# Optimization experiments

Measured on AMD Instinct MI355X. Metric: run time of the kernel, lower is better.

## Reference

```python
import jax, jax.numpy as jnp
import numpy as np

D_MODEL = 1024
NUM_HEADS = 16
D_K = D_MODEL // NUM_HEADS  # 64


def setup_inputs() -> dict:
    key = jax.random.key(0)
    k1, k2, k3, k4, k5 = jax.random.split(key, 5)
    scale = 1.0 / np.sqrt(D_MODEL)
    x = jax.random.normal(k1, (2, 8192, D_MODEL), dtype=jnp.float32)
    W_qkv = jax.random.normal(k2, (D_MODEL, 3 * D_MODEL), dtype=jnp.float32) * scale
    b_qkv = jax.random.normal(k3, (3 * D_MODEL,), dtype=jnp.float32) * 0.01
    W_out = jax.random.normal(k4, (D_MODEL, D_MODEL), dtype=jnp.float32) * scale
    b_out = jax.random.normal(k5, (D_MODEL,), dtype=jnp.float32) * 0.01
    return {"x": x, "W_qkv": W_qkv, "b_qkv": b_qkv, "W_out": W_out, "b_out": b_out}


def reference(x, W_qkv, b_qkv, W_out, b_out):
    B, S, _ = x.shape
    # qkv: [B, S, 3*d_model] -> reshape [B, S, H, 3*d_k] (matches torch reshape:
    # head h owns contiguous slice [h*3dk:(h+1)*3dk], split into q/k/v of d_k each)
    qkv = (jnp.einsum('bsd,de->bse', x, W_qkv) + b_qkv).reshape(B, S, NUM_HEADS, 3 * D_K)
    q, k, v = qkv[..., :D_K], qkv[..., D_K:2 * D_K], qkv[..., 2 * D_K:]
    # NOTE: faithful to source — no head transpose, so matmul contracts d_k and
    # produces scores across the HEAD axis: [B, S, H, H]
    scores = jnp.einsum('bshd,bsgd->bshg', q, k) / np.sqrt(D_K)
    attn = jax.nn.softmax(scores, axis=-1)  # softmax over heads (g)
    context = jnp.einsum('bshg,bsgd->bshd', attn, v).reshape(B, S, NUM_HEADS * D_K)
    return jnp.einsum('bsd,de->bse', context, W_out) + b_out
```

## Files before the change

kernel.cpp:

```cpp
#include <hip/hip_runtime.h>
#include <hip/hip_bf16.h>

typedef short bf16x8 __attribute__((ext_vector_type(8)));
typedef float f32x4 __attribute__((ext_vector_type(4)));
typedef ushort ushort8_t __attribute__((ext_vector_type(8)));

__device__ __forceinline__ float bf2f(ushort u) {
    union { unsigned int i; float f; } c; c.i = ((unsigned int)u) << 16; return c.f;
}
__device__ __forceinline__ ushort f2bf(float f) {
    union { float f; unsigned int i; } c; c.f = f;
    unsigned int x = c.i;
    return (ushort)((x + 0x7fffu + ((x >> 16) & 1u)) >> 16);
}

#define GLOAD_LDS16(g, l) __builtin_amdgcn_global_load_lds( \
    (const __attribute__((address_space(1))) unsigned int*)(g), \
    (__attribute__((address_space(3))) unsigned int*)(l), 16, 0, 0)

__global__ __launch_bounds__(256) void k_cvt_bf16(const float* __restrict__ in,
                                                  ushort* __restrict__ out, int n4) {
    int i = blockIdx.x * 256 + threadIdx.x;
    if (i < n4) {
        float4 v = ((const float4*)in)[i];
        ushort4 o;
        o.x = f2bf(v.x); o.y = f2bf(v.y); o.z = f2bf(v.z); o.w = f2bf(v.w);
        ((ushort4*)out)[i] = o;
    }
}

__global__ __launch_bounds__(256) void k_transpose_cvt(const float* __restrict__ in,
                                                       ushort* __restrict__ out,
                                                       int K, int N) {
    __shared__ float tile[32][33];
    int n0 = blockIdx.x * 32, k0 = blockIdx.y * 32;
    int tx = threadIdx.x, ty = threadIdx.y;
    #pragma unroll
    for (int i = 0; i < 32; i += 8)
        tile[ty + i][tx] = in[(size_t)(k0 + ty + i) * N + n0 + tx];
    __syncthreads();
    #pragma unroll
    for (int i = 0; i < 32; i += 8)
        out[(size_t)(n0 + ty + i) * K + k0 + tx] = f2bf(tile[tx][ty + i]);
}


#define LDSA(c,kk) (lds + (c)*65536 + (kk)*16384)
#define LDSB(c,kk) (lds + (c)*65536 + 32768 + (kk)*16384)
#define STAGE_A(c,kk,col) do { \
    GLOAD_LDS16(gA0 + (col), LDSA(c,kk) + wave*1024); \
    GLOAD_LDS16(gA1 + (col), LDSA(c,kk) + 8192 + wave*1024); } while(0)
#define STAGE_B(c,kk,col) do { \
    GLOAD_LDS16(gB0 + (col), LDSB(c,kk) + wave*1024); \
    GLOAD_LDS16(gB1 + (col), LDSB(c,kk) + 8192 + wave*1024); } while(0)
#define READ_AF(S,c,kk) do { const char* _p = LDSA(c,kk) + aoff; \
    _Pragma("unroll") for (int m = 0; m < 8; ++m) S[m] = *(const bf16x8*)(_p + m*1024); } while(0)
#define READ_B2(c,kk,n0) do { const char* _p = LDSB(c,kk) + boff; \
    bfr[n0] = *(const bf16x8*)(_p + (n0)*1024); \
    bfr[(n0)+1] = *(const bf16x8*)(_p + ((n0)+1)*1024); } while(0)
#define MF16(S,n0) do { __builtin_amdgcn_s_setprio(1); \
    _Pragma("unroll") for (int m = 0; m < 8; ++m) { \
    acc[m][n0]     = __builtin_amdgcn_mfma_f32_16x16x32_bf16(S[m], bfr[n0],     acc[m][n0],     0,0,0); \
    acc[m][(n0)+1] = __builtin_amdgcn_mfma_f32_16x16x32_bf16(S[m], bfr[(n0)+1], acc[m][(n0)+1], 0,0,0); } \
    __builtin_amdgcn_s_setprio(0); } while(0)

#define BAR __builtin_amdgcn_s_barrier()
#define SB0 __builtin_amdgcn_sched_barrier(0)
#define VM6 asm volatile("s_waitcnt vmcnt(6)")
#define VM0 asm volatile("s_waitcnt vmcnt(0)")

#define ITERX(kb, LAST) do { \
   READ_B2(0,0,2);                   STAGE_B(1,1,(kb)+96);              MF16(afA,0);                        BAR; SB0; \
   READ_AF(afB,0,1); READ_B2(0,1,0); if(!(LAST)) STAGE_A(0,0,(kb)+128); MF16(afA,2); VM6;                   BAR; SB0; \
   READ_B2(0,1,2);                   if(!(LAST)) STAGE_B(0,0,(kb)+128); MF16(afB,0);                        BAR; SB0; \
   READ_AF(afA,1,0); READ_B2(1,0,0); if(!(LAST)) STAGE_A(0,1,(kb)+160); MF16(afB,2); if(LAST) VM0; else VM6; BAR; SB0; \
   READ_B2(1,0,2);                   if(!(LAST)) STAGE_B(0,1,(kb)+160); MF16(afA,0);                        BAR; SB0; \
   READ_AF(afB,1,1); READ_B2(1,1,0); if(!(LAST)) STAGE_A(1,0,(kb)+192); MF16(afA,2); if(!(LAST)) VM6;       BAR; SB0; \
   READ_B2(1,1,2);                   if(!(LAST)) STAGE_B(1,0,(kb)+192); MF16(afB,0);                        BAR; SB0; \
   if(!(LAST)) { READ_AF(afA,0,0); READ_B2(0,0,0); STAGE_A(1,1,(kb)+224); } MF16(afB,2); if(!(LAST)) VM6;   BAR; SB0; \
} while(0)

template<bool OUT_BF16>
__global__ __launch_bounds__(512, 2) void k_gemm256(const ushort* __restrict__ A,
                                                    const ushort* __restrict__ Bt,
                                                    const float* __restrict__ bias,
                                                    void* __restrict__ Cout,
                                                    int N, int NTN) {
    __shared__ __align__(16) char lds[131072];
    const int K = 1024;
    const int tid = threadIdx.x;
    const int wave = tid >> 6, lane = tid & 63;
    const int wr = wave >> 2, wc = wave & 3;
    const int r = lane & 15, q = lane >> 4;

    const int cpx = gridDim.x >> 3, wg = blockIdx.x;
    const int swz = (wg & 7) * cpx + (wg >> 3);
    const int tm = swz / NTN, tn = swz - tm * NTN;
    const int bm = tm * 256, bn = tn * 256;

    const int srow = tid >> 2;
    const int c16l = (tid & 3) ^ ((srow >> 1) & 3);
    const ushort* gA0 = A  + (size_t)(bm + srow) * K + c16l * 8;
    const ushort* gA1 = gA0 + (size_t)128 * K;
    const ushort* gB0 = Bt + (size_t)(bn + srow) * K + c16l * 8;
    const ushort* gB1 = gB0 + (size_t)128 * K;

    const int chunkx = ((q ^ ((r >> 1) & 3)) << 4);
    const int aoff = (wr * 128 + r) * 64 + chunkx;
    const int boff = (wc * 64 + r) * 64 + chunkx;

    f32x4 acc[8][4];
    #pragma unroll
    for (int m = 0; m < 8; ++m)
        #pragma unroll
        for (int n = 0; n < 4; ++n)
            acc[m][n] = (f32x4){0.f, 0.f, 0.f, 0.f};
    bf16x8 afA[8], afB[8], bfr[4];

    STAGE_A(0,0,0);  STAGE_B(0,0,0);
    STAGE_A(0,1,32); STAGE_B(0,1,32);
    STAGE_A(1,0,64); STAGE_B(1,0,64);
    STAGE_A(1,1,96);
    VM6; BAR; SB0;
    READ_AF(afA,0,0); READ_B2(0,0,0);

    #pragma unroll 1
    for (int i = 0; i < 7; ++i) { ITERX(i * 128, 0); }
    ITERX(896, 1);

    float* Cf = (float*)Cout;
    ushort* Cb = (ushort*)Cout;
    #pragma unroll
    for (int m = 0; m < 8; ++m) {
        int row0 = bm + wr * 128 + m * 16 + q * 4;
        #pragma unroll
        for (int n = 0; n < 4; ++n) {
            int col = bn + wc * 64 + n * 16 + r;
            float bv = bias[col];
            #pragma unroll
            for (int j = 0; j < 4; ++j) {
                float v = acc[m][n][j] + bv;
                if (OUT_BF16) Cb[(size_t)(row0 + j) * N + col] = f2bf(v);
                else          Cf[(size_t)(row0 + j) * N + col] = v;
            }
        }
    }
}

__global__ __launch_bounds__(256) void k_attn_mfma(const ushort* __restrict__ qkv,
                                                   ushort* __restrict__ ctx) {
    const int lane = threadIdx.x & 63;
    const size_t tok = (size_t)blockIdx.x * 4 + (threadIdx.x >> 6);
    const ushort* row = qkv + tok * 3072;
    const int r = lane & 15, g = lane >> 4;

    bf16x8 ka[2], qb[2];
    #pragma unroll
    for (int c = 0; c < 2; ++c) {
        ka[c] = *(const bf16x8*)(row + r * 192 + 64 + c * 32 + g * 8);
        qb[c] = *(const bf16x8*)(row + r * 192 +      c * 32 + g * 8);
    }
    f32x4 st = (f32x4){0.f, 0.f, 0.f, 0.f};
    st = __builtin_amdgcn_mfma_f32_16x16x32_bf16(ka[0], qb[0], st, 0, 0, 0);
    st = __builtin_amdgcn_mfma_f32_16x16x32_bf16(ka[1], qb[1], st, 0, 0, 0);

    float s[4];
    #pragma unroll
    for (int j = 0; j < 4; ++j) s[j] = st[j] * 0.125f;
    float m = fmaxf(fmaxf(s[0], s[1]), fmaxf(s[2], s[3]));
    m = fmaxf(m, __shfl_xor(m, 16));
    m = fmaxf(m, __shfl_xor(m, 32));
    float p[4], sum = 0.f;
    #pragma unroll
    for (int j = 0; j < 4; ++j) { p[j] = __expf(s[j] - m); sum += p[j]; }
    sum += __shfl_xor(sum, 16);
    sum += __shfl_xor(sum, 32);
    float inv = 1.f / sum;
    #pragma unroll
    for (int j = 0; j < 4; ++j) p[j] *= inv;

    const bool gok = (g < 2);
    const int src0 = (r + 32 * g) & 63, src1 = (src0 + 16) & 63;
    bf16x8 pa;
    #pragma unroll
    for (int j = 0; j < 4; ++j) {
        float a0 = __shfl(p[j], src0, 64);
        float a1 = __shfl(p[j], src1, 64);
        pa[j]     = (short)(gok ? f2bf(a0) : (ushort)0);
        pa[4 + j] = (short)(gok ? f2bf(a1) : (ushort)0);
    }

    #pragma unroll
    for (int db = 0; db < 4; ++db) {
        bf16x8 vb;
        #pragma unroll
        for (int j = 0; j < 8; ++j)
            vb[j] = (short)(gok ? row[(g * 8 + j) * 192 + 128 + db * 16 + r] : (ushort)0);
        f32x4 o = (f32x4){0.f, 0.f, 0.f, 0.f};
        o = __builtin_amdgcn_mfma_f32_16x16x32_bf16(pa, vb, o, 0, 0, 0);
        #pragma unroll
        for (int j = 0; j < 4; ++j)
            ctx[tok * 1024 + (4 * g + j) * 64 + db * 16 + r] = f2bf(o[j]);
    }
}

extern "C" void kernel_launch(void* const* d_in, const int* in_sizes, int n_in,
                              void* d_out, int out_size, void* d_ws, size_t ws_size,
                              hipStream_t stream) {
    const float* x     = (const float*)d_in[0];
    const float* W_qkv = (const float*)d_in[1];
    const float* b_qkv = (const float*)d_in[2];
    const float* W_out = (const float*)d_in[3];
    const float* b_out = (const float*)d_in[4];

    const int M = 16384, D = 1024, N3 = 3072;

    ushort* xb   = (ushort*)d_ws;
    ushort* wqkT = xb + (size_t)M * D;
    ushort* woT  = wqkT + (size_t)N3 * D;
    ushort* qkv  = woT + (size_t)D * D;
    ushort* ctx  = xb;

    hipLaunchKernelGGL(k_cvt_bf16, dim3((M * D / 4 + 255) / 256), dim3(256), 0, stream,
                       x, xb, M * D / 4);
    hipLaunchKernelGGL(k_transpose_cvt, dim3(N3 / 32, D / 32), dim3(32, 8), 0, stream,
                       W_qkv, wqkT, D, N3);
    hipLaunchKernelGGL(k_transpose_cvt, dim3(D / 32, D / 32), dim3(32, 8), 0, stream,
                       W_out, woT, D, D);
    hipLaunchKernelGGL((k_gemm256<true>), dim3((N3 / 256) * (M / 256)), dim3(512), 0, stream,
                       xb, wqkT, b_qkv, (void*)qkv, N3, N3 / 256);
    hipLaunchKernelGGL(k_attn_mfma, dim3(M / 4), dim3(256), 0, stream, qkv, ctx);
    hipLaunchKernelGGL((k_gemm256<false>), dim3((D / 256) * (M / 256)), dim3(512), 0, stream,
                       ctx, woT, b_out, d_out, D, D / 256);
}
```

Before: 208.6 us.

## Single-buffer A fragments and restructure GEMM pipeline phases with relaxed vmcnt waits

```diff
diff --git a/kernel.cpp b/kernel.cpp
--- a/kernel.cpp
+++ b/kernel.cpp
@@ -53,31 +53,33 @@
 #define STAGE_B(c,kk,col) do { \
     GLOAD_LDS16(gB0 + (col), LDSB(c,kk) + wave*1024); \
     GLOAD_LDS16(gB1 + (col), LDSB(c,kk) + 8192 + wave*1024); } while(0)
-#define READ_AF(S,c,kk) do { const char* _p = LDSA(c,kk) + aoff; \
-    _Pragma("unroll") for (int m = 0; m < 8; ++m) S[m] = *(const bf16x8*)(_p + m*1024); } while(0)
+#define READ_A8(c,kk) do { const char* _p = LDSA(c,kk) + aoff; \
+    _Pragma("unroll") for (int m = 0; m < 8; ++m) af[m] = *(const bf16x8*)(_p + m*1024); } while(0)
 #define READ_B2(c,kk,n0) do { const char* _p = LDSB(c,kk) + boff; \
     bfr[n0] = *(const bf16x8*)(_p + (n0)*1024); \
     bfr[(n0)+1] = *(const bf16x8*)(_p + ((n0)+1)*1024); } while(0)
-#define MF16(S,n0) do { __builtin_amdgcn_s_setprio(1); \
+#define MF16(n0) do { __builtin_amdgcn_s_setprio(1); \
     _Pragma("unroll") for (int m = 0; m < 8; ++m) { \
-    acc[m][n0]     = __builtin_amdgcn_mfma_f32_16x16x32_bf16(S[m], bfr[n0],     acc[m][n0],     0,0,0); \
-    acc[m][(n0)+1] = __builtin_amdgcn_mfma_f32_16x16x32_bf16(S[m], bfr[(n0)+1], acc[m][(n0)+1], 0,0,0); } \
+    acc[m][n0]     = __builtin_amdgcn_mfma_f32_16x16x32_bf16(af[m], bfr[n0],     acc[m][n0],     0,0,0); \
+    acc[m][(n0)+1] = __builtin_amdgcn_mfma_f32_16x16x32_bf16(af[m], bfr[(n0)+1], acc[m][(n0)+1], 0,0,0); } \
     __builtin_amdgcn_s_setprio(0); } while(0)
 
 #define BAR __builtin_amdgcn_s_barrier()
 #define SB0 __builtin_amdgcn_sched_barrier(0)
-#define VM6 asm volatile("s_waitcnt vmcnt(6)")
-#define VM0 asm volatile("s_waitcnt vmcnt(0)")
+#define VM10 asm volatile("s_waitcnt vmcnt(10)")
+#define VM0  asm volatile("s_waitcnt vmcnt(0)")
+
+#define PH1(reads, stage, mf, vm) do { reads; stage; mf; SB0; vm; BAR; SB0; } while(0)
 
 #define ITERX(kb, LAST) do { \
-   READ_B2(0,0,2);                   STAGE_B(1,1,(kb)+96);              MF16(afA,0);                        BAR; SB0; \
-   READ_AF(afB,0,1); READ_B2(0,1,0); if(!(LAST)) STAGE_A(0,0,(kb)+128); MF16(afA,2); VM6;                   BAR; SB0; \
-   READ_B2(0,1,2);                   if(!(LAST)) STAGE_B(0,0,(kb)+128); MF16(afB,0);                        BAR; SB0; \
-   READ_AF(afA,1,0); READ_B2(1,0,0); if(!(LAST)) STAGE_A(0,1,(kb)+160); MF16(afB,2); if(LAST) VM0; else VM6; BAR; SB0; \
-   READ_B2(1,0,2);                   if(!(LAST)) STAGE_B(0,1,(kb)+160); MF16(afA,0);                        BAR; SB0; \
-   READ_AF(afB,1,1); READ_B2(1,1,0); if(!(LAST)) STAGE_A(1,0,(kb)+192); MF16(afA,2); if(!(LAST)) VM6;       BAR; SB0; \
-   READ_B2(1,1,2);                   if(!(LAST)) STAGE_B(1,0,(kb)+192); MF16(afB,0);                        BAR; SB0; \
-   if(!(LAST)) { READ_AF(afA,0,0); READ_B2(0,0,0); STAGE_A(1,1,(kb)+224); } MF16(afB,2); if(!(LAST)) VM6;   BAR; SB0; \
+   PH1( { READ_A8(0,0); READ_B2(0,0,0); }, STAGE_B(1,1,(kb)+96),              MF16(0), ); \
+   PH1( { READ_B2(0,0,2); },               if(!(LAST)) STAGE_A(0,0,(kb)+128), MF16(2), if(LAST) VM0; else VM10 ); \
+   PH1( { READ_A8(0,1); READ_B2(0,1,0); }, if(!(LAST)) STAGE_B(0,0,(kb)+128), MF16(0), ); \
+   PH1( { READ_B2(0,1,2); },               if(!(LAST)) STAGE_A(0,1,(kb)+160), MF16(2), if(!(LAST)) VM10 ); \
+   PH1( { READ_A8(1,0); READ_B2(1,0,0); }, if(!(LAST)) STAGE_B(0,1,(kb)+160), MF16(0), ); \
+   PH1( { READ_B2(1,0,2); },               if(!(LAST)) STAGE_A(1,0,(kb)+192), MF16(2), if(!(LAST)) VM10 ); \
+   PH1( { READ_A8(1,1); READ_B2(1,1,0); }, if(!(LAST)) STAGE_B(1,0,(kb)+192), MF16(0), ); \
+   PH1( { READ_B2(1,1,2); },               if(!(LAST)) STAGE_A(1,1,(kb)+224), MF16(2), if(!(LAST)) VM10 ); \
 } while(0)
 
 template<bool OUT_BF16>
@@ -115,14 +117,13 @@
         #pragma unroll
         for (int n = 0; n < 4; ++n)
             acc[m][n] = (f32x4){0.f, 0.f, 0.f, 0.f};
-    bf16x8 afA[8], afB[8], bfr[4];
+    bf16x8 af[8], bfr[4];
 
     STAGE_A(0,0,0);  STAGE_B(0,0,0);
     STAGE_A(0,1,32); STAGE_B(0,1,32);
     STAGE_A(1,0,64); STAGE_B(1,0,64);
     STAGE_A(1,1,96);
-    VM6; BAR; SB0;
-    READ_AF(afA,0,0); READ_B2(0,0,0);
+    VM10; BAR; SB0;
 
     #pragma unroll 1
     for (int i = 0; i < 7; ++i) { ITERX(i * 128, 0); }
```

After: 201.4 us. 3.5% less time.

## Restructure GEMM main loop into quadrant phases with two barriers per phase

Applied to the files above, without the earlier changes.

```diff
diff --git a/kernel.cpp b/kernel.cpp
--- a/kernel.cpp
+++ b/kernel.cpp
@@ -53,31 +53,41 @@
 #define STAGE_B(c,kk,col) do { \
     GLOAD_LDS16(gB0 + (col), LDSB(c,kk) + wave*1024); \
     GLOAD_LDS16(gB1 + (col), LDSB(c,kk) + 8192 + wave*1024); } while(0)
-#define READ_AF(S,c,kk) do { const char* _p = LDSA(c,kk) + aoff; \
-    _Pragma("unroll") for (int m = 0; m < 8; ++m) S[m] = *(const bf16x8*)(_p + m*1024); } while(0)
-#define READ_B2(c,kk,n0) do { const char* _p = LDSB(c,kk) + boff; \
-    bfr[n0] = *(const bf16x8*)(_p + (n0)*1024); \
-    bfr[(n0)+1] = *(const bf16x8*)(_p + ((n0)+1)*1024); } while(0)
-#define MF16(S,n0) do { __builtin_amdgcn_s_setprio(1); \
-    _Pragma("unroll") for (int m = 0; m < 8; ++m) { \
-    acc[m][n0]     = __builtin_amdgcn_mfma_f32_16x16x32_bf16(S[m], bfr[n0],     acc[m][n0],     0,0,0); \
-    acc[m][(n0)+1] = __builtin_amdgcn_mfma_f32_16x16x32_bf16(S[m], bfr[(n0)+1], acc[m][(n0)+1], 0,0,0); } \
+
+#define READ_A(c,MH) do { \
+    _Pragma("unroll") for (int m = 0; m < 4; ++m) { \
+        af[m*2+0] = *(const bf16x8*)(LDSA(c,0) + aoff + (MH)*4096 + m*1024); \
+        af[m*2+1] = *(const bf16x8*)(LDSA(c,1) + aoff + (MH)*4096 + m*1024); } } while(0)
+#define READ_B(c,NH,BR) do { \
+    _Pragma("unroll") for (int n = 0; n < 2; ++n) { \
+        BR[n*2+0] = *(const bf16x8*)(LDSB(c,0) + boff + (NH)*2048 + n*1024); \
+        BR[n*2+1] = *(const bf16x8*)(LDSB(c,1) + boff + (NH)*2048 + n*1024); } } while(0)
+#define MFQ(MH,NH,BR) do { __builtin_amdgcn_s_setprio(1); \
+    _Pragma("unroll") for (int m = 0; m < 4; ++m) \
+    _Pragma("unroll") for (int n = 0; n < 2; ++n) { \
+        f32x4 a = acc[(MH)*4+m][(NH)*2+n]; \
+        a = __builtin_amdgcn_mfma_f32_16x16x32_bf16(af[m*2+0], BR[n*2+0], a, 0,0,0); \
+        a = __builtin_amdgcn_mfma_f32_16x16x32_bf16(af[m*2+1], BR[n*2+1], a, 0,0,0); \
+        acc[(MH)*4+m][(NH)*2+n] = a; } \
     __builtin_amdgcn_s_setprio(0); } while(0)
 
 #define BAR __builtin_amdgcn_s_barrier()
 #define SB0 __builtin_amdgcn_sched_barrier(0)
-#define VM6 asm volatile("s_waitcnt vmcnt(6)")
+#define VM4 asm volatile("s_waitcnt vmcnt(4)")
 #define VM0 asm volatile("s_waitcnt vmcnt(0)")
 
-#define ITERX(kb, LAST) do { \
-   READ_B2(0,0,2);                   STAGE_B(1,1,(kb)+96);              MF16(afA,0);                        BAR; SB0; \
-   READ_AF(afB,0,1); READ_B2(0,1,0); if(!(LAST)) STAGE_A(0,0,(kb)+128); MF16(afA,2); VM6;                   BAR; SB0; \
-   READ_B2(0,1,2);                   if(!(LAST)) STAGE_B(0,0,(kb)+128); MF16(afB,0);                        BAR; SB0; \
-   READ_AF(afA,1,0); READ_B2(1,0,0); if(!(LAST)) STAGE_A(0,1,(kb)+160); MF16(afB,2); if(LAST) VM0; else VM6; BAR; SB0; \
-   READ_B2(1,0,2);                   if(!(LAST)) STAGE_B(0,1,(kb)+160); MF16(afA,0);                        BAR; SB0; \
-   READ_AF(afB,1,1); READ_B2(1,1,0); if(!(LAST)) STAGE_A(1,0,(kb)+192); MF16(afA,2); if(!(LAST)) VM6;       BAR; SB0; \
-   READ_B2(1,1,2);                   if(!(LAST)) STAGE_B(1,0,(kb)+192); MF16(afB,0);                        BAR; SB0; \
-   if(!(LAST)) { READ_AF(afA,0,0); READ_B2(0,0,0); STAGE_A(1,1,(kb)+224); } MF16(afB,2); if(!(LAST)) VM6;   BAR; SB0; \
+#define PH(reads, stage, mf, vm) do { reads; stage; BAR; \
+    asm volatile("s_waitcnt lgkmcnt(0)"); SB0; mf; vm; BAR; } while(0)
+
+#define ITERQ(kb, LAST) do { \
+  PH({READ_A(0,0); READ_B(0,0,bfrE);}, STAGE_A(1,1,(kb)+96),              MFQ(0,0,bfrE), ); \
+  PH({READ_B(0,1,bfrO);},              STAGE_B(1,1,(kb)+96),              MFQ(0,1,bfrO), ); \
+  PH({READ_A(0,1);},                   if(!(LAST)) STAGE_B(0,0,(kb)+128), MFQ(1,1,bfrO), ); \
+  PH({},                               if(!(LAST)) STAGE_A(0,0,(kb)+128), MFQ(1,0,bfrE), if(LAST) VM0; else VM4 ); \
+  PH({READ_A(1,0); READ_B(1,0,bfrE);}, if(!(LAST)) STAGE_B(0,1,(kb)+160), MFQ(0,0,bfrE), ); \
+  PH({READ_B(1,1,bfrO);},              if(!(LAST)) STAGE_A(0,1,(kb)+160), MFQ(0,1,bfrO), ); \
+  PH({READ_A(1,1);},                   if(!(LAST)) STAGE_B(1,0,(kb)+192), MFQ(1,1,bfrO), ); \
+  PH({},                               if(!(LAST)) STAGE_A(1,0,(kb)+192), MFQ(1,0,bfrE), if(!(LAST)) VM4 ); \
 } while(0)
 
 template<bool OUT_BF16>
@@ -115,18 +125,16 @@
         #pragma unroll
         for (int n = 0; n < 4; ++n)
             acc[m][n] = (f32x4){0.f, 0.f, 0.f, 0.f};
-    bf16x8 afA[8], afB[8], bfr[4];
-
-    STAGE_A(0,0,0);  STAGE_B(0,0,0);
-    STAGE_A(0,1,32); STAGE_B(0,1,32);
-    STAGE_A(1,0,64); STAGE_B(1,0,64);
-    STAGE_A(1,1,96);
-    VM6; BAR; SB0;
-    READ_AF(afA,0,0); READ_B2(0,0,0);
+    bf16x8 af[8], bfrE[4], bfrO[4];
+
+    STAGE_B(0,0,0);  STAGE_A(0,0,0);
+    STAGE_B(0,1,32); STAGE_A(0,1,32);
+    STAGE_B(1,0,64); STAGE_A(1,0,64);
+    VM4; BAR; SB0;
 
     #pragma unroll 1
-    for (int i = 0; i < 7; ++i) { ITERX(i * 128, 0); }
-    ITERX(896, 1);
+    for (int i = 0; i < 7; ++i) { ITERQ(i * 128, 0); }
+    ITERQ(896, 1);
 
     float* Cf = (float*)Cout;
     ushort* Cb = (ushort*)Cout;
```

After: 201.2 us. 1.04x faster.
